# Performance work log

Hardware: AMD Instinct MI355X
Metric: run time of the kernel (lower is better)

The kernel has to match this reference:

```python
import jax, jax.numpy as jnp
import numpy as np

MEMORY_COEF = 0.25
DHAT_COEF = 0.1

B, D, T, K = 64, 256, 512, 512
C, L = 8, 512


def setup_inputs() -> dict:
    key = jax.random.key(0)
    k1, k2, k3, k4, k5 = jax.random.split(key, 5)
    return {
        "Xhat": jax.random.normal(k1, (B, C, L), dtype=jnp.float32),
        "X": jax.random.normal(k2, (B, C, L), dtype=jnp.float32),
        "H": jax.random.normal(k3, (B, D, T), dtype=jnp.float32),
        "M": jax.random.normal(k4, (D, K), dtype=jnp.float32),
        "Dhat": jax.random.normal(k5, (B, T), dtype=jnp.float32),
    }


def _memory_loss(H, M):
    # H: [B, D, T]; M: [D, K] codebook with K codewords of dim D
    Ht = jnp.transpose(H, (0, 2, 1))  # [B, T, D]
    Mt = M.T                          # [K, D]
    # Squared distances via ||h||^2 - 2 h.m + ||m||^2 (argmin equals argmin of norms)
    d2 = (jnp.sum(Ht * Ht, axis=-1, keepdims=True)
          - 2.0 * jnp.einsum('btd,kd->btk', Ht, Mt)
          + jnp.sum(Mt * Mt, axis=-1))  # [B, T, K]
    idx = jnp.argmin(d2, axis=2)        # [B, T]
    Z = jnp.transpose(Mt[idx], (0, 2, 1))  # [B, D, T]
    sg = jax.lax.stop_gradient
    # ||.||^2 along dim D (norm then pow(2) == sum of squares)
    diffs = jnp.sum((sg(H) - Z) ** 2, axis=1) + jnp.sum((H - sg(Z)) ** 2, axis=1)  # [B, T]
    return jnp.sum(diffs) / float(np.prod(H.shape))


def reference(Xhat, X, H, M, Dhat):
    rec = jnp.mean((Xhat - X) ** 2)
    return rec + MEMORY_COEF * _memory_loss(H, M) - DHAT_COEF * jnp.mean(Dhat)
```

## Files before the change

kernel.cpp:

```cpp
#include <hip/hip_runtime.h>

#define NB   64
#define DD   256
#define TT   512
#define KK   512

typedef short bf8 __attribute__((ext_vector_type(8)));
typedef float f4  __attribute__((ext_vector_type(4)));

__device__ inline unsigned f2bf(float x) {
  unsigned u = __float_as_uint(x);
  u += 0x7FFFu + ((u >> 16) & 1u);
  return u >> 16;
}

#define MFMA(accv, va, vb) \
  asm("v_mfma_f32_16x16x32_bf16 %0, %1, %2, %0" : "+v"(accv) : "v"(va), "v"(vb))

#define ACCROW(acc, kt) \
    "+v"(acc[kt][0]), "+v"(acc[kt][1]), "+v"(acc[kt][2]), "+v"(acc[kt][3]), \
    "+v"(acc[kt][4]), "+v"(acc[kt][5]), "+v"(acc[kt][6]), "+v"(acc[kt][7])
#define ACCLIST8(acc) ACCROW(acc,0), ACCROW(acc,1), ACCROW(acc,2), ACCROW(acc,3)

__global__ __launch_bounds__(256) void edm_prep(
    const float* __restrict__ M, const float4* __restrict__ Xh,
    const float4* __restrict__ X, const float4* __restrict__ Dh,
    unsigned short* __restrict__ MtF, float* __restrict__ mnorm,
    float* __restrict__ recp, float* __restrict__ dhp,
    unsigned* __restrict__ counter) {
  __shared__ __align__(16) float tile[DD][68];
  __shared__ float pn[4][64];
  __shared__ float ps[8];

  const int bid  = blockIdx.x;
  const int tid  = threadIdx.x;
  const int lane = tid & 63;
  const int q    = tid >> 6;

  if (bid == 0 && tid == 0) *counter = 0u;

  if (bid < 8) {
    #pragma unroll
    for (int it = 0; it < 16; ++it) {
      const int d  = q * 64 + it * 4 + (lane >> 4);
      const int kc = (lane & 15) << 2;
      *(float4*)&tile[d][kc] = *(const float4*)(M + (size_t)d * KK + bid * 64 + kc);
    }
    __syncthreads();
    const int k    = bid * 64 + lane;
    const int k16  = k >> 4;
    const int r16k = k & 15;
    float s = 0.f;
    #pragma unroll
    for (int dsl = 0; dsl < 2; ++dsl) {
      const int ds = q * 2 + dsl;
      #pragma unroll
      for (int g = 0; g < 4; ++g) {
        unsigned pk[4];
        #pragma unroll
        for (int e = 0; e < 4; ++e) {
          const float x0 = tile[ds * 32 + g * 8 + 2 * e + 0][lane];
          const float x1 = tile[ds * 32 + g * 8 + 2 * e + 1][lane];
          s += x0 * x0 + x1 * x1;
          pk[e] = f2bf(x0) | (f2bf(x1) << 16);
        }
        *(uint4*)(MtF + ((size_t)(k16 * 8 + ds) * 64 + r16k + 16 * g) * 8) =
            make_uint4(pk[0], pk[1], pk[2], pk[3]);
      }
    }
    pn[q][lane] = s;
    __syncthreads();
    if (q == 0) mnorm[k] = pn[0][lane] + pn[1][lane] + pn[2][lane] + pn[3][lane];
  } else {
    const int r = bid - 8;
    float s = 0.f, sd = 0.f;
    #pragma unroll
    for (int i = 0; i < 4; ++i) {
      const int idx = r * 1024 + i * 256 + tid;
      const float4 a = Xh[idx];
      const float4 c = X[idx];
      const float e0 = a.x - c.x, e1 = a.y - c.y, e2 = a.z - c.z, e3 = a.w - c.w;
      s += e0 * e0 + e1 * e1 + e2 * e2 + e3 * e3;
    }
    if (tid < 128) {
      const float4 dd = Dh[r * 128 + tid];
      sd = dd.x + dd.y + dd.z + dd.w;
    }
    #pragma unroll
    for (int off = 32; off > 0; off >>= 1) {
      s  += __shfl_down(s, off);
      sd += __shfl_down(sd, off);
    }
    if (lane == 0) { ps[q] = s; ps[4 + q] = sd; }
    __syncthreads();
    if (tid == 0) {
      recp[r] = ps[0] + ps[1] + ps[2] + ps[3];
      dhp[r]  = ps[4] + ps[5] + ps[6] + ps[7];
    }
  }
}

__global__ __launch_bounds__(512, 2) void edm_main(
    const float* __restrict__ H, const unsigned short* __restrict__ MtF,
    const float* __restrict__ mnorm, const float* __restrict__ recp,
    const float* __restrict__ dhp, float* __restrict__ d2part,
    unsigned* __restrict__ counter, float* __restrict__ out) {
  __shared__ __align__(16) unsigned short Hbf[128 * 256];
  __shared__ float hsumP[4][128];
  __shared__ float wmin[8][128];
  __shared__ float red[12];
  __shared__ float bsum[2];
  __shared__ int   islast;

  const int tid  = threadIdx.x;
  const int wv   = tid >> 6;
  const int l    = tid & 63;
  const int tcol = tid & 127;
  const int q    = tid >> 7;
  const int r16  = l & 15;
  const int g    = l >> 4;

  const int b  = blockIdx.x >> 2;
  const int t0 = (blockIdx.x & 3) << 7;
  const float* Hcol = H + (size_t)b * DD * TT + t0 + tcol;

  float hacc = 0.f;
  char* rowp = (char*)Hbf + tcol * 512;
  const int swz = (tcol & 7) << 4;
  #pragma unroll
  for (int r = 0; r < 4; ++r) {
    float x[16];
    #pragma unroll
    for (int j = 0; j < 16; ++j)
      x[j] = Hcol[(size_t)(q * 64 + r * 16 + j) * TT];
    unsigned pk[8];
    #pragma unroll
    for (int e = 0; e < 8; ++e) {
      hacc += x[2 * e] * x[2 * e] + x[2 * e + 1] * x[2 * e + 1];
      pk[e] = f2bf(x[2 * e]) | (f2bf(x[2 * e + 1]) << 16);
    }
    const int dbyte = q * 128 + r * 32;
    *(uint4*)(rowp + ((dbyte +  0) ^ swz)) = make_uint4(pk[0], pk[1], pk[2], pk[3]);
    *(uint4*)(rowp + ((dbyte + 16) ^ swz)) = make_uint4(pk[4], pk[5], pk[6], pk[7]);
  }
  hsumP[q][tcol] = hacc;

  f4 acc[4][8];
  #pragma unroll
  for (int kt = 0; kt < 4; ++kt)
    #pragma unroll
    for (int tn = 0; tn < 8; ++tn)
      acc[kt][tn] = (f4){0.f, 0.f, 0.f, 0.f};
  asm volatile("s_nop 1" : ACCLIST8(acc));

  __syncthreads();

  #pragma unroll
  for (int ds = 0; ds < 8; ++ds) {
    bf8 afr[4];
    #pragma unroll
    for (int kt = 0; kt < 4; ++kt)
      afr[kt] = *(const bf8*)(MtF + (((size_t)(wv * 4 + kt) * 8 + ds) * 64 + l) * 8);
    #pragma unroll
    for (int tn = 0; tn < 8; ++tn) {
      const int t = tn * 16 + r16;
      const bf8 bfr = *(const bf8*)((const char*)Hbf + t * 512 +
                                    ((ds * 64 + g * 16) ^ ((t & 7) << 4)));
      MFMA(acc[0][tn], afr[0], bfr);
      MFMA(acc[1][tn], afr[1], bfr);
      MFMA(acc[2][tn], afr[2], bfr);
      MFMA(acc[3][tn], afr[3], bfr);
    }
  }
  asm volatile("s_nop 7\n\ts_nop 7" : ACCLIST8(acc));

  float rmin[8] = {3.0e38f, 3.0e38f, 3.0e38f, 3.0e38f,
                   3.0e38f, 3.0e38f, 3.0e38f, 3.0e38f};
  #pragma unroll
  for (int kt = 0; kt < 4; ++kt) {
    const f4 mn = *(const f4*)(mnorm + wv * 64 + kt * 16 + g * 4);
    #pragma unroll
    for (int tn = 0; tn < 8; ++tn) {
      #pragma unroll
      for (int rr = 0; rr < 4; ++rr)
        rmin[tn] = fminf(rmin[tn], mn[rr] - 2.f * acc[kt][tn][rr]);
    }
  }
  #pragma unroll
  for (int tn = 0; tn < 8; ++tn) {
    rmin[tn] = fminf(rmin[tn], __shfl_xor(rmin[tn], 16));
    rmin[tn] = fminf(rmin[tn], __shfl_xor(rmin[tn], 32));
  }
  if (g == 0) {
    #pragma unroll
    for (int tn = 0; tn < 8; ++tn) wmin[wv][tn * 16 + r16] = rmin[tn];
  }
  __syncthreads();

  if (tid < 128) {
    float m = wmin[0][tid];
    #pragma unroll
    for (int w = 1; w < 8; ++w) m = fminf(m, wmin[w][tid]);
    float v = m + hsumP[0][tid] + hsumP[1][tid] + hsumP[2][tid] + hsumP[3][tid];
    #pragma unroll
    for (int off = 32; off > 0; off >>= 1) v += __shfl_down(v, off);
    if ((tid & 63) == 0) bsum[tid >> 6] = v;
  }
  __syncthreads();
  if (tid == 0) {
    __hip_atomic_store(&d2part[blockIdx.x], bsum[0] + bsum[1],
                       __ATOMIC_RELEASE, __HIP_MEMORY_SCOPE_AGENT);
    islast = (__hip_atomic_fetch_add(counter, 1u, __ATOMIC_ACQ_REL,
                                     __HIP_MEMORY_SCOPE_AGENT) == 255u) ? 1 : 0;
  }
  __syncthreads();

  if (islast) {
    float a = 0.f, r = 0.f, dh = 0.f;
    if (tid < 256) {
      a = __hip_atomic_load(&d2part[tid], __ATOMIC_RELAXED,
                            __HIP_MEMORY_SCOPE_AGENT);
      if (tid < 64) { r = recp[tid]; dh = dhp[tid]; }
    }
    #pragma unroll
    for (int off = 32; off > 0; off >>= 1) {
      a  += __shfl_down(a, off);
      r  += __shfl_down(r, off);
      dh += __shfl_down(dh, off);
    }
    if (tid < 256 && (tid & 63) == 0) {
      const int w = tid >> 6;
      red[w] = a; red[4 + w] = r; red[8 + w] = dh;
    }
    __syncthreads();
    if (tid == 0) {
      const float d2sum  = red[0] + red[1] + red[2] + red[3];
      const float recsum = red[4] + red[5] + red[6] + red[7];
      const float dhsum  = red[8] + red[9] + red[10] + red[11];
      out[0] = recsum * (1.f / 262144.f)
             + d2sum  * (1.f / 16777216.f)
             - 0.1f * dhsum * (1.f / 32768.f);
    }
  }
}

extern "C" void kernel_launch(void* const* d_in, const int* in_sizes, int n_in,
                              void* d_out, int out_size, void* d_ws, size_t ws_size,
                              hipStream_t stream) {
  const float* Xh = (const float*)d_in[0];
  const float* X  = (const float*)d_in[1];
  const float* H  = (const float*)d_in[2];
  const float* M  = (const float*)d_in[3];
  const float* Dh = (const float*)d_in[4];
  float* out = (float*)d_out;

  unsigned short* MtF = (unsigned short*)d_ws;
  float* mnorm = (float*)((char*)d_ws + (size_t)KK * DD * 2);
  float* recp  = mnorm + KK;
  float* dhp   = recp + 64;
  float* d2p   = dhp + 64;
  unsigned* counter = (unsigned*)(d2p + 256);

  edm_prep<<<72, 256, 0, stream>>>(M, (const float4*)Xh, (const float4*)X,
                                   (const float4*)Dh, MtF, mnorm, recp, dhp,
                                   counter);
  edm_main<<<NB * (TT / 128), 512, 0, stream>>>(H, MtF, mnorm, recp, dhp,
                                                d2p, counter, out);
}
```

Baseline: 28.70 us.

## Fuse prep kernel into main kernel, converting codebook to bf16 on the fly

```diff
diff --git a/kernel.cpp b/kernel.cpp
--- a/kernel.cpp
+++ b/kernel.cpp
@@ -8,11 +8,7 @@
 typedef short bf8 __attribute__((ext_vector_type(8)));
 typedef float f4  __attribute__((ext_vector_type(4)));
 
-__device__ inline unsigned f2bf(float x) {
-  unsigned u = __float_as_uint(x);
-  u += 0x7FFFu + ((u >> 16) & 1u);
-  return u >> 16;
-}
+union BF8U { bf8 v; unsigned u[4]; };
 
 #define MFMA(accv, va, vb) \
   asm("v_mfma_f32_16x16x32_bf16 %0, %1, %2, %0" : "+v"(accv) : "v"(va), "v"(vb))
@@ -22,128 +18,86 @@
     "+v"(acc[kt][4]), "+v"(acc[kt][5]), "+v"(acc[kt][6]), "+v"(acc[kt][7])
 #define ACCLIST8(acc) ACCROW(acc,0), ACCROW(acc,1), ACCROW(acc,2), ACCROW(acc,3)
 
-__global__ __launch_bounds__(256) void edm_prep(
-    const float* __restrict__ M, const float4* __restrict__ Xh,
-    const float4* __restrict__ X, const float4* __restrict__ Dh,
-    unsigned short* __restrict__ MtF, float* __restrict__ mnorm,
-    float* __restrict__ recp, float* __restrict__ dhp,
-    unsigned* __restrict__ counter) {
-  __shared__ __align__(16) float tile[DD][68];
-  __shared__ float pn[4][64];
-  __shared__ float ps[8];
-
-  const int bid  = blockIdx.x;
-  const int tid  = threadIdx.x;
-  const int lane = tid & 63;
-  const int q    = tid >> 6;
-
-  if (bid == 0 && tid == 0) *counter = 0u;
-
-  if (bid < 8) {
-    #pragma unroll
-    for (int it = 0; it < 16; ++it) {
-      const int d  = q * 64 + it * 4 + (lane >> 4);
-      const int kc = (lane & 15) << 2;
-      *(float4*)&tile[d][kc] = *(const float4*)(M + (size_t)d * KK + bid * 64 + kc);
-    }
-    __syncthreads();
-    const int k    = bid * 64 + lane;
-    const int k16  = k >> 4;
-    const int r16k = k & 15;
-    float s = 0.f;
-    #pragma unroll
-    for (int dsl = 0; dsl < 2; ++dsl) {
-      const int ds = q * 2 + dsl;
-      #pragma unroll
-      for (int g = 0; g < 4; ++g) {
-        unsigned pk[4];
-        #pragma unroll
-        for (int e = 0; e < 4; ++e) {
-          const float x0 = tile[ds * 32 + g * 8 + 2 * e + 0][lane];
-          const float x1 = tile[ds * 32 + g * 8 + 2 * e + 1][lane];
-          s += x0 * x0 + x1 * x1;
-          pk[e] = f2bf(x0) | (f2bf(x1) << 16);
-        }
-        *(uint4*)(MtF + ((size_t)(k16 * 8 + ds) * 64 + r16k + 16 * g) * 8) =
-            make_uint4(pk[0], pk[1], pk[2], pk[3]);
-      }
-    }
-    pn[q][lane] = s;
-    __syncthreads();
-    if (q == 0) mnorm[k] = pn[0][lane] + pn[1][lane] + pn[2][lane] + pn[3][lane];
-  } else {
-    const int r = bid - 8;
-    float s = 0.f, sd = 0.f;
-    #pragma unroll
-    for (int i = 0; i < 4; ++i) {
-      const int idx = r * 1024 + i * 256 + tid;
-      const float4 a = Xh[idx];
-      const float4 c = X[idx];
-      const float e0 = a.x - c.x, e1 = a.y - c.y, e2 = a.z - c.z, e3 = a.w - c.w;
-      s += e0 * e0 + e1 * e1 + e2 * e2 + e3 * e3;
-    }
-    if (tid < 128) {
-      const float4 dd = Dh[r * 128 + tid];
-      sd = dd.x + dd.y + dd.z + dd.w;
-    }
-    #pragma unroll
-    for (int off = 32; off > 0; off >>= 1) {
-      s  += __shfl_down(s, off);
-      sd += __shfl_down(sd, off);
-    }
-    if (lane == 0) { ps[q] = s; ps[4 + q] = sd; }
-    __syncthreads();
-    if (tid == 0) {
-      recp[r] = ps[0] + ps[1] + ps[2] + ps[3];
-      dhp[r]  = ps[4] + ps[5] + ps[6] + ps[7];
-    }
-  }
-}
-
-__global__ __launch_bounds__(512, 2) void edm_main(
-    const float* __restrict__ H, const unsigned short* __restrict__ MtF,
-    const float* __restrict__ mnorm, const float* __restrict__ recp,
-    const float* __restrict__ dhp, float* __restrict__ d2part,
-    unsigned* __restrict__ counter, float* __restrict__ out) {
+__device__ inline unsigned pkbf(float x0, float x1, unsigned sel) {
+  const unsigned a = __float_as_uint(x0) + 0x8000u;
+  const unsigned b = __float_as_uint(x1) + 0x8000u;
+  unsigned d;
+  asm("v_perm_b32 %0, %1, %2, %3" : "=v"(d) : "v"(b), "v"(a), "s"(sel));
+  return d;
+}
+
+__device__ inline void lgkm_barrier() {
+  asm volatile("s_waitcnt lgkmcnt(0)" ::: "memory");
+  __builtin_amdgcn_s_barrier();
+  asm volatile("" ::: "memory");
+}
+
+__global__ __launch_bounds__(512, 2) void edm_all(
+    const float* __restrict__ H, const float* __restrict__ M,
+    const float4* __restrict__ Xh, const float4* __restrict__ X,
+    const float4* __restrict__ Dh,
+    float* __restrict__ d2part, unsigned* __restrict__ counter,
+    float* __restrict__ out) {
   __shared__ __align__(16) unsigned short Hbf[128 * 256];
+  __shared__ __align__(16) float mn_lds[512];
   __shared__ float hsumP[4][128];
   __shared__ float wmin[8][128];
+  __shared__ float recw[4], dhw[4];
   __shared__ float red[12];
   __shared__ float bsum[2];
   __shared__ int   islast;
 
   const int tid  = threadIdx.x;
+  const int bid  = blockIdx.x;
   const int wv   = tid >> 6;
   const int l    = tid & 63;
   const int tcol = tid & 127;
   const int q    = tid >> 7;
   const int r16  = l & 15;
   const int g    = l >> 4;
-
-  const int b  = blockIdx.x >> 2;
-  const int t0 = (blockIdx.x & 3) << 7;
+  const unsigned sel = 0x07060302u;
+
+  const int b  = bid >> 2;
+  const int t0 = (bid & 3) << 7;
   const float* Hcol = H + (size_t)b * DD * TT + t0 + tcol;
 
-  float hacc = 0.f;
+  float recv = 0.f, dhv = 0.f;
+  if (tid < 256) {
+    const float4 a = Xh[bid * 256 + tid];
+    const float4 c = X[bid * 256 + tid];
+    const float e0 = a.x - c.x, e1 = a.y - c.y, e2 = a.z - c.z, e3 = a.w - c.w;
+    recv = e0 * e0 + e1 * e1 + e2 * e2 + e3 * e3;
+    if (tid < 32) {
+      const float4 dd = Dh[bid * 32 + tid];
+      dhv = dd.x + dd.y + dd.z + dd.w;
+    }
+  }
+
   char* rowp = (char*)Hbf + tcol * 512;
   const int swz = (tcol & 7) << 4;
-  #pragma unroll
-  for (int r = 0; r < 4; ++r) {
-    float x[16];
-    #pragma unroll
-    for (int j = 0; j < 16; ++j)
-      x[j] = Hcol[(size_t)(q * 64 + r * 16 + j) * TT];
-    unsigned pk[8];
-    #pragma unroll
-    for (int e = 0; e < 8; ++e) {
-      hacc += x[2 * e] * x[2 * e] + x[2 * e + 1] * x[2 * e + 1];
-      pk[e] = f2bf(x[2 * e]) | (f2bf(x[2 * e + 1]) << 16);
-    }
-    const int dbyte = q * 128 + r * 32;
-    *(uint4*)(rowp + ((dbyte +  0) ^ swz)) = make_uint4(pk[0], pk[1], pk[2], pk[3]);
-    *(uint4*)(rowp + ((dbyte + 16) ^ swz)) = make_uint4(pk[4], pk[5], pk[6], pk[7]);
-  }
-  hsumP[q][tcol] = hacc;
+  float hacc = 0.f;
+
+  #define PACKSTORE(xarr, dbyte)                                              \
+    { unsigned pk[8];                                                         \
+      _Pragma("unroll")                                                       \
+      for (int e = 0; e < 8; ++e) {                                           \
+        hacc += xarr[2*e] * xarr[2*e] + xarr[2*e+1] * xarr[2*e+1];            \
+        pk[e] = pkbf(xarr[2*e], xarr[2*e+1], sel);                            \
+      }                                                                       \
+      *(uint4*)(rowp + (((dbyte) +  0) ^ swz)) = make_uint4(pk[0],pk[1],pk[2],pk[3]); \
+      *(uint4*)(rowp + (((dbyte) + 16) ^ swz)) = make_uint4(pk[4],pk[5],pk[6],pk[7]); }
+
+  float xA[16], xB[16], xC[16], xD[16];
+  #pragma unroll
+  for (int j = 0; j < 16; ++j) xA[j] = Hcol[(size_t)(      q * 16 + j) * TT];
+  #pragma unroll
+  for (int j = 0; j < 16; ++j) xB[j] = Hcol[(size_t)( 64 + q * 16 + j) * TT];
+  PACKSTORE(xA, q * 32)
+  PACKSTORE(xB, 128 + q * 32)
+  #pragma unroll
+  for (int j = 0; j < 16; ++j) xC[j] = Hcol[(size_t)(128 + q * 16 + j) * TT];
+  #pragma unroll
+  for (int j = 0; j < 16; ++j) xD[j] = Hcol[(size_t)(192 + q * 16 + j) * TT];
 
   f4 acc[4][8];
   #pragma unroll
@@ -153,32 +107,76 @@
       acc[kt][tn] = (f4){0.f, 0.f, 0.f, 0.f};
   asm volatile("s_nop 1" : ACCLIST8(acc));
 
-  __syncthreads();
-
-  #pragma unroll
-  for (int ds = 0; ds < 8; ++ds) {
-    bf8 afr[4];
-    #pragma unroll
-    for (int kt = 0; kt < 4; ++kt)
-      afr[kt] = *(const bf8*)(MtF + (((size_t)(wv * 4 + kt) * 8 + ds) * 64 + l) * 8);
-    #pragma unroll
-    for (int tn = 0; tn < 8; ++tn) {
-      const int t = tn * 16 + r16;
-      const bf8 bfr = *(const bf8*)((const char*)Hbf + t * 512 +
-                                    ((ds * 64 + g * 16) ^ ((t & 7) << 4)));
-      MFMA(acc[0][tn], afr[0], bfr);
-      MFMA(acc[1][tn], afr[1], bfr);
-      MFMA(acc[2][tn], afr[2], bfr);
-      MFMA(acc[3][tn], afr[3], bfr);
-    }
-  }
+  lgkm_barrier();
+
+  const float* Mb = M + (size_t)(g * 8) * KK + wv * 64 + r16;
+  float msq[4] = {0.f, 0.f, 0.f, 0.f};
+
+  #define MFMA_HALF(h)                                                        \
+    _Pragma("unroll")                                                         \
+    for (int s = 0; s < 4; ++s) {                                             \
+      const int ds = (h) * 4 + s;                                             \
+      BF8U afr[4];                                                            \
+      _Pragma("unroll")                                                       \
+      for (int kt = 0; kt < 4; ++kt) {                                        \
+        float mx[8];                                                          \
+        _Pragma("unroll")                                                     \
+        for (int j = 0; j < 8; ++j)                                           \
+          mx[j] = Mb[(size_t)(ds * 32 + j) * KK + kt * 16];                   \
+        _Pragma("unroll")                                                     \
+        for (int j = 0; j < 8; ++j) msq[kt] += mx[j] * mx[j];                 \
+        afr[kt].u[0] = pkbf(mx[0], mx[1], sel);                               \
+        afr[kt].u[1] = pkbf(mx[2], mx[3], sel);                               \
+        afr[kt].u[2] = pkbf(mx[4], mx[5], sel);                               \
+        afr[kt].u[3] = pkbf(mx[6], mx[7], sel);                               \
+      }                                                                       \
+      asm volatile("s_nop 2" : "+v"(afr[0].v), "+v"(afr[1].v),                \
+                               "+v"(afr[2].v), "+v"(afr[3].v));               \
+      _Pragma("unroll")                                                       \
+      for (int tn = 0; tn < 8; ++tn) {                                        \
+        const int t = tn * 16 + r16;                                          \
+        const bf8 bfr = *(const bf8*)((const char*)Hbf + t * 512 +            \
+                            ((ds * 64 + g * 16) ^ ((t & 7) << 4)));           \
+        MFMA(acc[0][tn], afr[0].v, bfr);                                      \
+        MFMA(acc[1][tn], afr[1].v, bfr);                                      \
+        MFMA(acc[2][tn], afr[2].v, bfr);                                      \
+        MFMA(acc[3][tn], afr[3].v, bfr);                                      \
+      }                                                                       \
+    }
+
+  MFMA_HALF(0)
+
+  PACKSTORE(xC, 256 + q * 32)
+  PACKSTORE(xD, 384 + q * 32)
+  hsumP[q][tcol] = hacc;
+  lgkm_barrier();
+
+  MFMA_HALF(1)
   asm volatile("s_nop 7\n\ts_nop 7" : ACCLIST8(acc));
+
+  #pragma unroll
+  for (int kt = 0; kt < 4; ++kt) {
+    float v = msq[kt];
+    v += __shfl_xor(v, 16);
+    v += __shfl_xor(v, 32);
+    if (g == 0) mn_lds[wv * 64 + kt * 16 + r16] = v;
+  }
+  {
+    float rsum = recv, dsum = dhv;
+    #pragma unroll
+    for (int off = 32; off > 0; off >>= 1) {
+      rsum += __shfl_down(rsum, off);
+      dsum += __shfl_down(dsum, off);
+    }
+    if (tid < 256 && l == 0) { recw[wv] = rsum; dhw[wv] = dsum; }
+  }
+  __syncthreads();
 
   float rmin[8] = {3.0e38f, 3.0e38f, 3.0e38f, 3.0e38f,
                    3.0e38f, 3.0e38f, 3.0e38f, 3.0e38f};
   #pragma unroll
   for (int kt = 0; kt < 4; ++kt) {
-    const f4 mn = *(const f4*)(mnorm + wv * 64 + kt * 16 + g * 4);
+    const f4 mn = *(const f4*)&mn_lds[wv * 64 + kt * 16 + g * 4];
     #pragma unroll
     for (int tn = 0; tn < 8; ++tn) {
       #pragma unroll
@@ -207,40 +205,31 @@
     if ((tid & 63) == 0) bsum[tid >> 6] = v;
   }
   __syncthreads();
+
   if (tid == 0) {
-    __hip_atomic_store(&d2part[blockIdx.x], bsum[0] + bsum[1],
-                       __ATOMIC_RELEASE, __HIP_MEMORY_SCOPE_AGENT);
-    islast = (__hip_atomic_fetch_add(counter, 1u, __ATOMIC_ACQ_REL,
-                                     __HIP_MEMORY_SCOPE_AGENT) == 255u) ? 1 : 0;
+    const float rsumT = recw[0] + recw[1] + recw[2] + recw[3];
+    const float dsumT = dhw[0] + dhw[1] + dhw[2] + dhw[3];
+    const float contrib = (bsum[0] + bsum[1]) * (1.f / 16777216.f)
+                        + rsumT * (1.f / 262144.f)
+                        - 0.1f * dsumT * (1.f / 32768.f);
+    __hip_atomic_store(&d2part[bid], contrib, __ATOMIC_RELEASE,
+                       __HIP_MEMORY_SCOPE_AGENT);
+    const unsigned old = __hip_atomic_fetch_add(counter, 1u, __ATOMIC_ACQ_REL,
+                                                __HIP_MEMORY_SCOPE_AGENT);
+    islast = (old == 255u) ? 1 : 0;
   }
   __syncthreads();
 
   if (islast) {
-    float a = 0.f, r = 0.f, dh = 0.f;
-    if (tid < 256) {
+    float a = 0.f;
+    if (tid < 256)
       a = __hip_atomic_load(&d2part[tid], __ATOMIC_RELAXED,
                             __HIP_MEMORY_SCOPE_AGENT);
-      if (tid < 64) { r = recp[tid]; dh = dhp[tid]; }
-    }
-    #pragma unroll
-    for (int off = 32; off > 0; off >>= 1) {
-      a  += __shfl_down(a, off);
-      r  += __shfl_down(r, off);
-      dh += __shfl_down(dh, off);
-    }
-    if (tid < 256 && (tid & 63) == 0) {
-      const int w = tid >> 6;
-      red[w] = a; red[4 + w] = r; red[8 + w] = dh;
-    }
+    #pragma unroll
+    for (int off = 32; off > 0; off >>= 1) a += __shfl_down(a, off);
+    if (tid < 256 && l == 0) red[wv] = a;
     __syncthreads();
-    if (tid == 0) {
-      const float d2sum  = red[0] + red[1] + red[2] + red[3];
-      const float recsum = red[4] + red[5] + red[6] + red[7];
-      const float dhsum  = red[8] + red[9] + red[10] + red[11];
-      out[0] = recsum * (1.f / 262144.f)
-             + d2sum  * (1.f / 16777216.f)
-             - 0.1f * dhsum * (1.f / 32768.f);
-    }
+    if (tid == 0) out[0] = red[0] + red[1] + red[2] + red[3];
   }
 }
 
@@ -254,16 +243,12 @@
   const float* Dh = (const float*)d_in[4];
   float* out = (float*)d_out;
 
-  unsigned short* MtF = (unsigned short*)d_ws;
-  float* mnorm = (float*)((char*)d_ws + (size_t)KK * DD * 2);
-  float* recp  = mnorm + KK;
-  float* dhp   = recp + 64;
-  float* d2p   = dhp + 64;
-  unsigned* counter = (unsigned*)(d2p + 256);
-
-  edm_prep<<<72, 256, 0, stream>>>(M, (const float4*)Xh, (const float4*)X,
-                                   (const float4*)Dh, MtF, mnorm, recp, dhp,
-                                   counter);
-  edm_main<<<NB * (TT / 128), 512, 0, stream>>>(H, MtF, mnorm, recp, dhp,
-                                                d2p, counter, out);
-}
+  float* d2part     = (float*)d_ws;
+  unsigned* counter = (unsigned*)(d2part + 256);
+
+  hipMemsetAsync(counter, 0, sizeof(unsigned), stream);
+
+  edm_all<<<NB * (TT / 128), 512, 0, stream>>>(
+      H, M, (const float4*)Xh, (const float4*)X, (const float4*)Dh,
+      d2part, counter, out);
+}
```

Result: slower. 62.33 us (+117.2%).
